# Optimization experiments

Measured on AMD Instinct MI355X. Metric: run time of the kernel, lower is better.

Reference implementation:

```python
import jax, jax.numpy as jnp
import numpy as np
from jax import lax


def _quadrature_weights(bw):
    # s2cnn-style Driscoll-Healy quadrature weights over beta, length 2*bw
    j = np.arange(2 * bw)
    k = np.arange(bw)
    theta = np.pi * (2 * j + 1) / (4 * bw)
    s = (np.sin(np.outer(2 * j + 1, 2 * k + 1) * np.pi / (4 * bw)) / (2 * k + 1)).sum(-1)
    return jnp.asarray((2.0 / bw) * np.sin(theta) * s, jnp.float32)


def _conv2d(x, W, b):
    y = lax.conv_general_dilated(x, W, (1, 1), 'SAME',
                                 dimension_numbers=('NCHW', 'OIHW', 'NCHW'))
    return y + b[None, :, None, None]


def setup_inputs() -> dict:
    key = jax.random.key(0)
    ks = jax.random.split(key, 8)
    b, n = 8, 32768
    res_pt, res_r = 32, 8
    inputs = jax.random.normal(ks[0], (b, n, 3), jnp.float32)
    return {
        'inputs': inputs,
        'scale': jnp.float32(3.0),      # max radius covered by radial bins
        'sigma': jnp.float32(0.5),      # gaussian width in grid units
        'A': jnp.float32(1.0),          # splat amplitude
        'inteval_comp': jnp.float32(0.5),
        'res_pt': res_pt,
        'res_r': res_r,
        'W_s2_1': 0.08 * jax.random.normal(ks[1], (32, 8, 3, 3), jnp.float32),
        'b_s2_1': jnp.zeros((32,), jnp.float32),
        'W_s2_2': 0.05 * jax.random.normal(ks[2], (64, 32, 3, 3), jnp.float32),
        'b_s2_2': jnp.zeros((64,), jnp.float32),
        'W_gamma': 0.1 * jax.random.normal(ks[3], (64, 32), jnp.float32),
        'W_c3_1': 0.05 * jax.random.normal(ks[4], (64, 128), jnp.float32),
        'b_c3_1': jnp.zeros((64,), jnp.float32),
        'W_c3_2': 0.05 * jax.random.normal(ks[5], (32, 64), jnp.float32),
        'b_c3_2': jnp.zeros((32,), jnp.float32),
    }


def reference(inputs, scale, sigma, A, inteval_comp, res_pt, res_r,
              W_s2_1, b_s2_1, W_s2_2, b_s2_2, W_gamma,
              W_c3_1, b_c3_1, W_c3_2, b_c3_2):
    b, n, _ = inputs.shape
    # ---- remap: cartesian -> spherical with min-radius clamp (utils.remap) ----
    x, y, z = inputs[..., 0], inputs[..., 1], inputs[..., 2]
    r = jnp.maximum(jnp.sqrt(x * x + y * y + z * z), 0.1)
    theta = jnp.arccos(jnp.clip(z / r, -1.0, 1.0))            # [0, pi]
    phi = jnp.arctan2(y, x) + np.pi                            # [0, 2pi)
    # ---- s2_gridding: gaussian-weighted point -> (theta,phi,r) grid scatter ----
    ct = theta / np.pi * res_pt                                # continuous bin coords
    cp = phi / (2 * np.pi) * res_pt
    cr = r / scale * res_r
    it = jnp.clip(jnp.floor(ct).astype(jnp.int32), 0, res_pt - 1)
    ip = jnp.clip(jnp.floor(cp).astype(jnp.int32), 0, res_pt - 1)
    ir = jnp.clip(jnp.floor(cr).astype(jnp.int32), 0, res_r - 1)
    d2 = ((ct - (it + inteval_comp)) ** 2
          + (cp - (ip + inteval_comp)) ** 2
          + (cr - (ir + inteval_comp)) ** 2)
    w = A * jnp.exp(-d2 / (2.0 * sigma * sigma))               # (b, n)
    vals = jnp.stack([w, w * x, w * y, w * z], axis=-1)        # (b, n, 4)
    bidx = jnp.arange(b, dtype=jnp.int32)[:, None] * jnp.ones((1, n), jnp.int32)
    flat = ((bidx * res_pt + it) * res_pt + ip) * res_r + ir   # (b, n)
    grid = jnp.zeros((b * res_pt * res_pt * res_r, 4), jnp.float32)
    grid = grid.at[flat.reshape(-1)].add(vals.reshape(-1, 4))
    grid = grid.reshape(b, res_pt, res_pt, res_r, 4)
    ft = jnp.transpose(grid[..., 0], (0, 3, 1, 2))             # (b, res_r, res_pt, res_pt)
    # ---- encoder_l1 (s2cnn_equators): S2 convs + gamma lift to SO3 grid ----
    h = jax.nn.relu(_conv2d(ft, W_s2_1, b_s2_1))
    h = jax.nn.relu(_conv2d(h, W_s2_2, b_s2_2))                # (b, 64, res_pt, res_pt)
    ft_grid = jnp.einsum('bcxy,cg->bcxyg', h, W_gamma)         # (b, 64, rp, rp, rp)
    # ---- so3_integrate: quadrature weight over beta, sum alpha/gamma ----
    wq = _quadrature_weights(res_pt // 2)                      # (res_pt,)
    ft_max = jnp.einsum('bcxyg,y->bc', ft_grid, wq)            # (b, 64)
    # ---- broadcast global feature, concat, pointwise conv3d head ----
    ft_max_ = jnp.broadcast_to(ft_max[:, :, None, None, None],
                               (b, ft_grid.shape[1], res_pt, res_pt, res_pt))
    cat = jnp.concatenate([ft_grid, ft_max_], axis=1)          # (b, 128, rp, rp, rp)
    h3 = jax.nn.relu(jnp.einsum('bcxyg,dc->bdxyg', cat, W_c3_1)
                     + b_c3_1[None, :, None, None, None])
    out = (jnp.einsum('bdxyg,ed->bexyg', h3, W_c3_2)
           + b_c3_2[None, :, None, None, None])                # (b, 32, rp, rp, rp)
    ft_g = out.reshape(b, out.shape[1], -1).max(-1)            # (b, 32)
    return (out, ft_g)
```

## Files before the change

kernel.cpp:

```cpp
#include <hip/hip_runtime.h>
#include <math.h>

#define PI_D 3.14159265358979323846
#define PI_F 3.14159265358979323846f

typedef _Float16 half8 __attribute__((ext_vector_type(8)));
typedef _Float16 half4v __attribute__((ext_vector_type(4)));
typedef float floatx4 __attribute__((ext_vector_type(4)));
#define MFMA16(a,b,c) __builtin_amdgcn_mfma_f32_16x16x32_f16(a,b,c,0,0,0)

__global__ void k_prep(const float* __restrict__ Wg, const float* __restrict__ Wc31,
                       const float* __restrict__ Wc32,
                       _Float16* __restrict__ VswH, _Float16* __restrict__ VswL,
                       _Float16* __restrict__ W2swH, _Float16* __restrict__ W2swL,
                       float* __restrict__ ft, float* __restrict__ WS,
                       float* __restrict__ wq, float* __restrict__ sgs) {
  int flat = blockIdx.x * 256 + threadIdx.x;
  {
    int jj = flat & 7;
    int l  = (flat >> 3) & 63;
    int rest = flat >> 9;
    int ks = rest & 1, mt = rest >> 1;
    int c = ks*32 + (l >> 4)*8 + jj;
    int m = mt*16 + (l & 15);
    int g = m >> 6, d = m & 63;
    float val = Wg[c*32 + g] * Wc31[d*128 + c];
    _Float16 hi = (_Float16)val;
    VswH[flat] = hi;
    VswL[flat] = (_Float16)(val - (float)hi);
  }
  if (flat < 2048) {
    int jj = flat & 7;
    int l  = (flat >> 3) & 63;
    int rest = flat >> 9;
    int ks = rest & 1, mt2 = rest >> 1;
    int e = mt2*16 + (l & 15);
    int d = ks*32 + (l >> 4)*8 + jj;
    float val = Wc32[e*64 + d];
    _Float16 hi = (_Float16)val;
    W2swH[flat] = hi;
    W2swL[flat] = (_Float16)(val - (float)hi);
  }
  if (flat < 16384) ((float4*)ft)[flat] = make_float4(0.f, 0.f, 0.f, 0.f);
  if (flat < 32) {
    double jj = 2.0*(double)flat + 1.0;
    double theta = PI_D * jj / 64.0;
    double s = 0.0;
    for (int k = 0; k < 16; ++k)
      s += sin(jj * (double)(2*k+1) * PI_D / 64.0) / (double)(2*k+1);
    wq[flat] = (float)((2.0/16.0) * sin(theta) * s);
  } else if (flat < 96) {
    int c = flat - 32;
    float s = 0.f;
    for (int g = 0; g < 32; ++g) s += Wg[c*32 + g];
    sgs[c] = s;
  } else if (flat < 608) {
    WS[flat - 96] = 0.f;
  }
}

__global__ void k_scatter(const float* __restrict__ inp,
                          const float* __restrict__ p_scale,
                          const float* __restrict__ p_sigma,
                          const float* __restrict__ p_A,
                          const float* __restrict__ p_ic,
                          float* __restrict__ ft) {
  int i = blockIdx.x * 256 + threadIdx.x;
  float scale = p_scale[0];
  float sigma = p_sigma[0];
  float A     = p_A[0];
  float icomp = p_ic[0];
  int b = i >> 15;
  float x = inp[i*3+0];
  float y = inp[i*3+1];
  float z = inp[i*3+2];
  float r = sqrtf(x*x + y*y + z*z);
  r = fmaxf(r, 0.1f);
  float ctv = fminf(fmaxf(z / r, -1.0f), 1.0f);
  float theta = acosf(ctv);
  float phi = atan2f(y, x) + PI_F;
  float ct = theta * (32.0f / PI_F);
  float cp = phi * (32.0f / (2.0f * PI_F));
  float cr = r / scale * 8.0f;
  int it = (int)floorf(ct); it = min(max(it, 0), 31);
  int ip = (int)floorf(cp); ip = min(max(ip, 0), 31);
  int ir = (int)floorf(cr); ir = min(max(ir, 0), 7);
  float dt = ct - ((float)it + icomp);
  float dp = cp - ((float)ip + icomp);
  float dr = cr - ((float)ir + icomp);
  float d2 = dt*dt + dp*dp + dr*dr;
  float w = A * expf(-d2 / (2.0f * sigma * sigma));
  atomicAdd(&ft[((b*8 + ir)*32 + it)*32 + ip], w);
}

__global__ __launch_bounds__(512) void k_conv12(
    const float* __restrict__ ft, const float* __restrict__ W1,
    const float* __restrict__ b1, const float* __restrict__ W2,
    const float* __restrict__ b2, const float* __restrict__ wq,
    float* __restrict__ h2, float* __restrict__ WS) {
  __shared__ __align__(16) float ftt[8][5][32];
  __shared__ __align__(16) float h1t[32][3][32];
  __shared__ __align__(16) float W1s[72*32];
  __shared__ __align__(16) float W2s[288*64];
  int blk = blockIdx.x;
  int b = blk >> 5, xt = blk & 31;
  int t = threadIdx.x;

  for (int idx = t; idx < 2304; idx += 512) {
    int oc2 = idx & 31, rest = idx >> 5;
    W1s[rest*32 + oc2] = W1[oc2*72 + rest];
  }
  for (int idx = t; idx < 18432; idx += 512) {
    int oc = idx & 63, rest = idx >> 6;
    W2s[rest*64 + oc] = W2[oc*288 + rest];
  }
  for (int idx = t; idx < 1280; idx += 512) {
    int y = idx & 31, xx = (idx >> 5) % 5, ic = idx / 160;
    int xg = xt + xx - 2;
    ftt[ic][xx][y] = ((unsigned)xg < 32u) ? ft[b*8192 + ic*1024 + xg*32 + y] : 0.f;
  }
  __syncthreads();

  {
    int y = t & 31, grp = t >> 5;
    float acc[2][3];
    float bb0 = b1[grp*2+0], bb1 = b1[grp*2+1];
#pragma unroll
    for (int xr = 0; xr < 3; ++xr) { acc[0][xr] = bb0; acc[1][xr] = bb1; }
    for (int ic = 0; ic < 8; ++ic) {
      float v[5][3];
#pragma unroll
      for (int dyi = 0; dyi < 3; ++dyi) {
        int yy = y + dyi - 1;
        bool ok = ((unsigned)yy < 32u);
        int yc = min(max(yy, 0), 31);
#pragma unroll
        for (int xx = 0; xx < 5; ++xx) {
          float tv = ftt[ic][xx][yc];
          v[xx][dyi] = ok ? tv : 0.f;
        }
      }
#pragma unroll
      for (int k = 0; k < 9; ++k) {
        float2 w = *(const float2*)&W1s[(ic*9 + k)*32 + grp*2];
        int dx = k / 3, dy = k % 3;
#pragma unroll
        for (int xr = 0; xr < 3; ++xr) {
          float vv = v[xr + dx][dy];
          acc[0][xr] = fmaf(vv, w.x, acc[0][xr]);
          acc[1][xr] = fmaf(vv, w.y, acc[1][xr]);
        }
      }
    }
#pragma unroll
    for (int xr = 0; xr < 3; ++xr) {
      int xg = xt + xr - 1;
      bool ok = ((unsigned)xg < 32u);
      h1t[grp*2+0][xr][y] = ok ? fmaxf(acc[0][xr], 0.f) : 0.f;
      h1t[grp*2+1][xr][y] = ok ? fmaxf(acc[1][xr], 0.f) : 0.f;
    }
  }
  __syncthreads();

  {
    int y = t & 31, og = t >> 5, oc0 = og*4;
    float a0 = b2[oc0+0], a1 = b2[oc0+1], a2 = b2[oc0+2], a3 = b2[oc0+3];
    for (int ic2 = 0; ic2 < 32; ++ic2) {
      float v[3][3];
#pragma unroll
      for (int dyi = 0; dyi < 3; ++dyi) {
        int yy = y + dyi - 1;
        bool ok = ((unsigned)yy < 32u);
        int yc = min(max(yy, 0), 31);
#pragma unroll
        for (int xxi = 0; xxi < 3; ++xxi) {
          float tv = h1t[ic2][xxi][yc];
          v[xxi][dyi] = ok ? tv : 0.f;
        }
      }
#pragma unroll
      for (int k = 0; k < 9; ++k) {
        float4 w = *(const float4*)&W2s[(ic2*9 + k)*64 + oc0];
        float vv = v[k/3][k%3];
        a0 = fmaf(vv, w.x, a0);
        a1 = fmaf(vv, w.y, a1);
        a2 = fmaf(vv, w.z, a2);
        a3 = fmaf(vv, w.w, a3);
      }
    }
    float r0 = fmaxf(a0, 0.f), r1 = fmaxf(a1, 0.f);
    float r2 = fmaxf(a2, 0.f), r3 = fmaxf(a3, 0.f);
    int pp = xt*32 + y;
    h2[(b*64 + oc0+0)*1024 + pp] = r0;
    h2[(b*64 + oc0+1)*1024 + pp] = r1;
    h2[(b*64 + oc0+2)*1024 + pp] = r2;
    h2[(b*64 + oc0+3)*1024 + pp] = r3;
    float wqv = wq[y];
    float s0 = r0*wqv, s1 = r1*wqv, s2 = r2*wqv, s3 = r3*wqv;
#pragma unroll
    for (int m = 1; m < 32; m <<= 1) {
      s0 += __shfl_xor(s0, m, 64);
      s1 += __shfl_xor(s1, m, 64);
      s2 += __shfl_xor(s2, m, 64);
      s3 += __shfl_xor(s3, m, 64);
    }
    if ((t & 31) == 0) {
      atomicAdd(&WS[b*64 + oc0+0], s0);
      atomicAdd(&WS[b*64 + oc0+1], s1);
      atomicAdd(&WS[b*64 + oc0+2], s2);
      atomicAdd(&WS[b*64 + oc0+3], s3);
    }
  }
}

__global__ __launch_bounds__(512, 4) void k_head(
    const float* __restrict__ h2, const float* __restrict__ WS,
    const float* __restrict__ sgs,
    const float* __restrict__ Wc31, const float* __restrict__ bc31,
    const float* __restrict__ bc32,
    const half8* __restrict__ VswH, const half8* __restrict__ VswL,
    const half8* __restrict__ W2swH, const half8* __restrict__ W2swL,
    float* __restrict__ out, float* __restrict__ blockmax) {
  __shared__ __align__(16) _Float16 h3H[512*72];
  __shared__ float Ks[64];
  __shared__ float vbuf2[128];
  int blk = blockIdx.x;
  int b = blk >> 6, x = (blk >> 1) & 31, h = blk & 1;
  int t = threadIdx.x;
  int lane = t & 63, w = t >> 6;
  int n16 = lane & 15, quad = lane >> 4;

  if (t < 64) {
    float acc = bc31[t];
    const float* wr = Wc31 + t*128 + 64;
    const float* wsb = WS + b*64;
    for (int c = 0; c < 64; ++c)
      acc = fmaf(wr[c], sgs[c]*wsb[c], acc);
    Ks[t] = acc;
  }

  half8 bh00, bh01, bh10, bh11, bl00, bl01, bl10, bl11;
  {
    const float* h2b = h2 + (size_t)b*64*1024 + x*32;
#pragma unroll
    for (int j = 0; j < 8; ++j) {
      int c0 = quad*8 + j;
      int c1 = 32 + c0;
      float f00 = h2b[c0*1024 + n16];
      float f01 = h2b[c1*1024 + n16];
      float f10 = h2b[c0*1024 + 16 + n16];
      float f11 = h2b[c1*1024 + 16 + n16];
      _Float16 g00 = (_Float16)f00, g01 = (_Float16)f01;
      _Float16 g10 = (_Float16)f10, g11 = (_Float16)f11;
      bh00[j] = g00;  bl00[j] = (_Float16)(f00 - (float)g00);
      bh01[j] = g01;  bl01[j] = (_Float16)(f01 - (float)g01);
      bh10[j] = g10;  bl10[j] = (_Float16)(f10 - (float)g10);
      bh11[j] = g11;  bl11[j] = (_Float16)(f11 - (float)g11);
    }
  }
  int mt2 = w & 1;
  half8 a2h0 = W2swH[(mt2*2 + 0)*64 + lane];
  half8 a2h1 = W2swH[(mt2*2 + 1)*64 + lane];
  half8 a2l0 = W2swL[(mt2*2 + 0)*64 + lane];
  half8 a2l1 = W2swL[(mt2*2 + 1)*64 + lane];
  float bias_e[4];
#pragma unroll
  for (int r = 0; r < 4; ++r) bias_e[r] = bc32[mt2*16 + quad*4 + r];
  __syncthreads();

  for (int i = 0; i < 8; ++i) {
    int mt = h*64 + w*8 + i;
    half8 ah0 = VswH[(mt*2 + 0)*64 + lane];
    half8 ah1 = VswH[(mt*2 + 1)*64 + lane];
    half8 al0 = VswL[(mt*2 + 0)*64 + lane];
    half8 al1 = VswL[(mt*2 + 1)*64 + lane];
    floatx4 acc0 = {0.f, 0.f, 0.f, 0.f};
    floatx4 acc1 = {0.f, 0.f, 0.f, 0.f};
    acc0 = MFMA16(ah0, bh00, acc0);  acc1 = MFMA16(ah0, bh10, acc1);
    acc0 = MFMA16(ah0, bl00, acc0);  acc1 = MFMA16(ah0, bl10, acc1);
    acc0 = MFMA16(al0, bh00, acc0);  acc1 = MFMA16(al0, bh10, acc1);
    acc0 = MFMA16(ah1, bh01, acc0);  acc1 = MFMA16(ah1, bh11, acc1);
    acc0 = MFMA16(ah1, bl01, acc0);  acc1 = MFMA16(ah1, bl11, acc1);
    acc0 = MFMA16(al1, bh01, acc0);  acc1 = MFMA16(al1, bh11, acc1);
    int g = mt >> 2, gl = g & 15;
    int dbase = (mt & 3)*16 + quad*4;
    float4 kv = *(const float4*)&Ks[dbase];
#pragma unroll
    for (int nt = 0; nt < 2; ++nt) {
      floatx4 a = nt ? acc1 : acc0;
      int y = nt*16 + n16;
      int rowc = y*16 + gl;
      int dsw = (dbase + y*8) & 63;
      half4v hv;
      hv[0] = (_Float16)fmaxf(a[0] + kv.x, 0.f);
      hv[1] = (_Float16)fmaxf(a[1] + kv.y, 0.f);
      hv[2] = (_Float16)fmaxf(a[2] + kv.z, 0.f);
      hv[3] = (_Float16)fmaxf(a[3] + kv.w, 0.f);
      *(half4v*)&h3H[rowc*72 + dsw] = hv;
    }
  }
  __syncthreads();
  float vmax[4] = {-3.4e38f, -3.4e38f, -3.4e38f, -3.4e38f};
  for (int i = 0; i < 8; ++i) {
    int nt2 = (w >> 1)*8 + i;
    int rowc = nt2*16 + n16;
    int dsw0 = (quad*8 + nt2*8) & 63;
    int dsw1 = (32 + quad*8 + nt2*8) & 63;
    half8 b2h0 = *(const half8*)&h3H[rowc*72 + dsw0];
    half8 b2h1 = *(const half8*)&h3H[rowc*72 + dsw1];
    floatx4 acc = {0.f, 0.f, 0.f, 0.f};
    acc = MFMA16(a2h0, b2h0, acc);
    acc = MFMA16(a2l0, b2h0, acc);
    acc = MFMA16(a2h1, b2h1, acc);
    acc = MFMA16(a2l1, b2h1, acc);
    int y = nt2, g = h*16 + n16;
    size_t base = (((size_t)(b*32 + mt2*16 + quad*4))*1024 + (size_t)(x*32 + y))*32 + g;
#pragma unroll
    for (int r = 0; r < 4; ++r) {
      float v = acc[r] + bias_e[r];
      out[base + (size_t)r*32768] = v;
      vmax[r] = fmaxf(vmax[r], v);
    }
  }
#pragma unroll
  for (int m = 1; m < 16; m <<= 1) {
#pragma unroll
    for (int r = 0; r < 4; ++r)
      vmax[r] = fmaxf(vmax[r], __shfl_xor(vmax[r], m, 64));
  }
  if (n16 == 0) {
#pragma unroll
    for (int r = 0; r < 4; ++r) vbuf2[w*16 + quad*4 + r] = vmax[r];
  }
  __syncthreads();
  if (t < 32) {
    int e = t, m2 = e >> 4, el = e & 15;
    float mm = fmaxf(fmaxf(vbuf2[(m2+0)*16 + el], vbuf2[(m2+2)*16 + el]),
                     fmaxf(vbuf2[(m2+4)*16 + el], vbuf2[(m2+6)*16 + el]));
    blockmax[blk*32 + e] = mm;
  }
}

__global__ void k_final(const float* __restrict__ blockmax, float* __restrict__ ftg) {
  int t = threadIdx.x;
  int b = t >> 5, e = t & 31;
  float m = -3.4e38f;
  for (int s = 0; s < 64; ++s) m = fmaxf(m, blockmax[(b*64 + s)*32 + e]);
  ftg[b*32 + e] = m;
}

extern "C" void kernel_launch(void* const* d_in, const int* in_sizes, int n_in,
                              void* d_out, int out_size, void* d_ws, size_t ws_size,
                              hipStream_t stream) {
  const float* inputs = (const float*)d_in[0];
  const float* scale  = (const float*)d_in[1];
  const float* sigma  = (const float*)d_in[2];
  const float* A      = (const float*)d_in[3];
  const float* icmp   = (const float*)d_in[4];
  const float* W1   = (const float*)d_in[7];
  const float* b1   = (const float*)d_in[8];
  const float* W2   = (const float*)d_in[9];
  const float* b2   = (const float*)d_in[10];
  const float* Wg   = (const float*)d_in[11];
  const float* Wc31 = (const float*)d_in[12];
  const float* bc31 = (const float*)d_in[13];
  const float* Wc32 = (const float*)d_in[14];
  const float* bc32 = (const float*)d_in[15];

  float* ws    = (float*)d_ws;
  float* ft    = ws;
  float* h2    = ws + 327680;
  float* WS    = ws + 851968;
  float* bmax  = ws + 852480;
  float* wq    = ws + 868864;
  float* sgs   = ws + 868896;
  _Float16* VswH  = (_Float16*)(ws + 868992);
  _Float16* VswL  = (_Float16*)(ws + 934528);
  _Float16* W2swH = (_Float16*)(ws + 1000064);
  _Float16* W2swL = (_Float16*)(ws + 1001088);
  float* out   = (float*)d_out;
  float* ftg   = out + 8388608;

  k_prep<<<512, 256, 0, stream>>>(Wg, Wc31, Wc32, VswH, VswL, W2swH, W2swL,
                                  ft, WS, wq, sgs);
  k_scatter<<<1024, 256, 0, stream>>>(inputs, scale, sigma, A, icmp, ft);
  k_conv12<<<256, 512, 0, stream>>>(ft, W1, b1, W2, b2, wq, h2, WS);
  k_head<<<512, 512, 0, stream>>>(h2, WS, sgs, Wc31, bc31, bc32,
                                  (const half8*)VswH, (const half8*)VswL,
                                  (const half8*)W2swH, (const half8*)W2swL,
                                  out, bmax);
  k_final<<<1, 256, 0, stream>>>(bmax, ftg);
}
```

Before: 175.5 us.

## Fold prep kernel into scatter/conv, pad LDS weights, split head blocks finer

Removes the separate k_prep launch. The ft buffer is now zeroed with a memset, the small setup work moves into block 0 of k_scatter, and the fp16 weight swizzling moves into k_conv12. Conv weights are now loaded from global memory coalesced and stored in LDS with padded strides (33/65) to avoid bank conflicts, at the cost of giving up vector LDS reads. k_head is split into 1024 blocks, each handling half the y range with half the LDS, and launch bounds rise to 8 blocks per SM for more occupancy. The final reduction and workspace offsets are adjusted to match.

```diff
diff --git a/kernel.cpp b/kernel.cpp
--- a/kernel.cpp
+++ b/kernel.cpp
@@ -8,64 +8,34 @@
 typedef _Float16 half4v __attribute__((ext_vector_type(4)));
 typedef float floatx4 __attribute__((ext_vector_type(4)));
 #define MFMA16(a,b,c) __builtin_amdgcn_mfma_f32_16x16x32_f16(a,b,c,0,0,0)
-
-__global__ void k_prep(const float* __restrict__ Wg, const float* __restrict__ Wc31,
-                       const float* __restrict__ Wc32,
-                       _Float16* __restrict__ VswH, _Float16* __restrict__ VswL,
-                       _Float16* __restrict__ W2swH, _Float16* __restrict__ W2swL,
-                       float* __restrict__ ft, float* __restrict__ WS,
-                       float* __restrict__ wq, float* __restrict__ sgs) {
-  int flat = blockIdx.x * 256 + threadIdx.x;
-  {
-    int jj = flat & 7;
-    int l  = (flat >> 3) & 63;
-    int rest = flat >> 9;
-    int ks = rest & 1, mt = rest >> 1;
-    int c = ks*32 + (l >> 4)*8 + jj;
-    int m = mt*16 + (l & 15);
-    int g = m >> 6, d = m & 63;
-    float val = Wg[c*32 + g] * Wc31[d*128 + c];
-    _Float16 hi = (_Float16)val;
-    VswH[flat] = hi;
-    VswL[flat] = (_Float16)(val - (float)hi);
-  }
-  if (flat < 2048) {
-    int jj = flat & 7;
-    int l  = (flat >> 3) & 63;
-    int rest = flat >> 9;
-    int ks = rest & 1, mt2 = rest >> 1;
-    int e = mt2*16 + (l & 15);
-    int d = ks*32 + (l >> 4)*8 + jj;
-    float val = Wc32[e*64 + d];
-    _Float16 hi = (_Float16)val;
-    W2swH[flat] = hi;
-    W2swL[flat] = (_Float16)(val - (float)hi);
-  }
-  if (flat < 16384) ((float4*)ft)[flat] = make_float4(0.f, 0.f, 0.f, 0.f);
-  if (flat < 32) {
-    double jj = 2.0*(double)flat + 1.0;
-    double theta = PI_D * jj / 64.0;
-    double s = 0.0;
-    for (int k = 0; k < 16; ++k)
-      s += sin(jj * (double)(2*k+1) * PI_D / 64.0) / (double)(2*k+1);
-    wq[flat] = (float)((2.0/16.0) * sin(theta) * s);
-  } else if (flat < 96) {
-    int c = flat - 32;
-    float s = 0.f;
-    for (int g = 0; g < 32; ++g) s += Wg[c*32 + g];
-    sgs[c] = s;
-  } else if (flat < 608) {
-    WS[flat - 96] = 0.f;
-  }
-}
 
 __global__ void k_scatter(const float* __restrict__ inp,
                           const float* __restrict__ p_scale,
                           const float* __restrict__ p_sigma,
                           const float* __restrict__ p_A,
                           const float* __restrict__ p_ic,
-                          float* __restrict__ ft) {
-  int i = blockIdx.x * 256 + threadIdx.x;
+                          const float* __restrict__ Wg,
+                          float* __restrict__ ft, float* __restrict__ wq,
+                          float* __restrict__ sgs, float* __restrict__ WS) {
+  int blk = blockIdx.x, t = threadIdx.x;
+  if (blk == 0) {
+    if (t < 32) {
+      double jj = 2.0*(double)t + 1.0;
+      double theta = PI_D * jj / 64.0;
+      double s = 0.0;
+      for (int k = 0; k < 16; ++k)
+        s += sin(jj * (double)(2*k+1) * PI_D / 64.0) / (double)(2*k+1);
+      wq[t] = (float)((2.0/16.0) * sin(theta) * s);
+    } else if (t < 96) {
+      int c = t - 32;
+      float s = 0.f;
+      for (int g = 0; g < 32; ++g) s += Wg[c*32 + g];
+      sgs[c] = s;
+    } else if (t < 224) {
+      ((float4*)WS)[t - 96] = make_float4(0.f, 0.f, 0.f, 0.f);
+    }
+  }
+  int i = blk * 256 + t;
   float scale = p_scale[0];
   float sigma = p_sigma[0];
   float A     = p_A[0];
@@ -97,22 +67,55 @@
     const float* __restrict__ ft, const float* __restrict__ W1,
     const float* __restrict__ b1, const float* __restrict__ W2,
     const float* __restrict__ b2, const float* __restrict__ wq,
+    const float* __restrict__ Wg, const float* __restrict__ Wc31,
+    const float* __restrict__ Wc32,
+    _Float16* __restrict__ VswH, _Float16* __restrict__ VswL,
+    _Float16* __restrict__ W2swH, _Float16* __restrict__ W2swL,
     float* __restrict__ h2, float* __restrict__ WS) {
   __shared__ __align__(16) float ftt[8][5][32];
   __shared__ __align__(16) float h1t[32][3][32];
-  __shared__ __align__(16) float W1s[72*32];
-  __shared__ __align__(16) float W2s[288*64];
+  __shared__ __align__(16) float W1s[72*33];
+  __shared__ __align__(16) float W2s[288*65];
   int blk = blockIdx.x;
   int b = blk >> 5, xt = blk & 31;
   int t = threadIdx.x;
 
+  {
+    int flat = blk * 512 + t;
+    int jj = flat & 7;
+    int l  = (flat >> 3) & 63;
+    int rest = flat >> 9;
+    int ks = rest & 1, mt = rest >> 1;
+    int c = ks*32 + (l >> 4)*8 + jj;
+    int m = mt*16 + (l & 15);
+    int g = m >> 6, d = m & 63;
+    float val = Wg[c*32 + g] * Wc31[d*128 + c];
+    _Float16 hi = (_Float16)val;
+    VswH[flat] = hi;
+    VswL[flat] = (_Float16)(val - (float)hi);
+    if (flat < 2048) {
+      int ks2 = rest & 1, mt2 = rest >> 1;
+      int e = mt2*16 + (l & 15);
+      int dd = ks2*32 + (l >> 4)*8 + jj;
+      float v2 = Wc32[e*64 + dd];
+      _Float16 h2i = (_Float16)v2;
+      W2swH[flat] = h2i;
+      W2swL[flat] = (_Float16)(v2 - (float)h2i);
+    }
+  }
+
   for (int idx = t; idx < 2304; idx += 512) {
-    int oc2 = idx & 31, rest = idx >> 5;
-    W1s[rest*32 + oc2] = W1[oc2*72 + rest];
-  }
-  for (int idx = t; idx < 18432; idx += 512) {
-    int oc = idx & 63, rest = idx >> 6;
-    W2s[rest*64 + oc] = W2[oc*288 + rest];
+    int oc2 = idx / 72, rest = idx % 72;
+    W1s[rest*33 + oc2] = W1[idx];
+  }
+  for (int idx = t; idx < 4608; idx += 512) {
+    float4 v4 = ((const float4*)W2)[idx];
+    int base = idx * 4;
+    int oc = base / 288, r0 = base % 288;
+    W2s[(r0+0)*65 + oc] = v4.x;
+    W2s[(r0+1)*65 + oc] = v4.y;
+    W2s[(r0+2)*65 + oc] = v4.z;
+    W2s[(r0+3)*65 + oc] = v4.w;
   }
   for (int idx = t; idx < 1280; idx += 512) {
     int y = idx & 31, xx = (idx >> 5) % 5, ic = idx / 160;
@@ -142,13 +145,14 @@
       }
 #pragma unroll
       for (int k = 0; k < 9; ++k) {
-        float2 w = *(const float2*)&W1s[(ic*9 + k)*32 + grp*2];
+        float w0 = W1s[(ic*9 + k)*33 + grp*2];
+        float w1 = W1s[(ic*9 + k)*33 + grp*2 + 1];
         int dx = k / 3, dy = k % 3;
 #pragma unroll
         for (int xr = 0; xr < 3; ++xr) {
           float vv = v[xr + dx][dy];
-          acc[0][xr] = fmaf(vv, w.x, acc[0][xr]);
-          acc[1][xr] = fmaf(vv, w.y, acc[1][xr]);
+          acc[0][xr] = fmaf(vv, w0, acc[0][xr]);
+          acc[1][xr] = fmaf(vv, w1, acc[1][xr]);
         }
       }
     }
@@ -180,12 +184,13 @@
       }
 #pragma unroll
       for (int k = 0; k < 9; ++k) {
-        float4 w = *(const float4*)&W2s[(ic2*9 + k)*64 + oc0];
+        int row = (ic2*9 + k)*65 + oc0;
+        float w0 = W2s[row+0], w1 = W2s[row+1], w2 = W2s[row+2], w3 = W2s[row+3];
         float vv = v[k/3][k%3];
-        a0 = fmaf(vv, w.x, a0);
-        a1 = fmaf(vv, w.y, a1);
-        a2 = fmaf(vv, w.z, a2);
-        a3 = fmaf(vv, w.w, a3);
+        a0 = fmaf(vv, w0, a0);
+        a1 = fmaf(vv, w1, a1);
+        a2 = fmaf(vv, w2, a2);
+        a3 = fmaf(vv, w3, a3);
       }
     }
     float r0 = fmaxf(a0, 0.f), r1 = fmaxf(a1, 0.f);
@@ -213,7 +218,7 @@
   }
 }
 
-__global__ __launch_bounds__(512, 4) void k_head(
+__global__ __launch_bounds__(512, 8) void k_head(
     const float* __restrict__ h2, const float* __restrict__ WS,
     const float* __restrict__ sgs,
     const float* __restrict__ Wc31, const float* __restrict__ bc31,
@@ -221,11 +226,11 @@
     const half8* __restrict__ VswH, const half8* __restrict__ VswL,
     const half8* __restrict__ W2swH, const half8* __restrict__ W2swL,
     float* __restrict__ out, float* __restrict__ blockmax) {
-  __shared__ __align__(16) _Float16 h3H[512*72];
+  __shared__ __align__(16) _Float16 h3H[256*72];
   __shared__ float Ks[64];
   __shared__ float vbuf2[128];
   int blk = blockIdx.x;
-  int b = blk >> 6, x = (blk >> 1) & 31, h = blk & 1;
+  int b = blk >> 7, x = (blk >> 2) & 31, h = (blk >> 1) & 1, yh = blk & 1;
   int t = threadIdx.x;
   int lane = t & 63, w = t >> 6;
   int n16 = lane & 15, quad = lane >> 4;
@@ -239,23 +244,17 @@
     Ks[t] = acc;
   }
 
-  half8 bh00, bh01, bh10, bh11, bl00, bl01, bl10, bl11;
+  half8 bh0, bh1, bl0, bl1;
   {
-    const float* h2b = h2 + (size_t)b*64*1024 + x*32;
+    const float* h2b = h2 + (size_t)b*64*1024 + x*32 + yh*16;
 #pragma unroll
     for (int j = 0; j < 8; ++j) {
       int c0 = quad*8 + j;
-      int c1 = 32 + c0;
-      float f00 = h2b[c0*1024 + n16];
-      float f01 = h2b[c1*1024 + n16];
-      float f10 = h2b[c0*1024 + 16 + n16];
-      float f11 = h2b[c1*1024 + 16 + n16];
-      _Float16 g00 = (_Float16)f00, g01 = (_Float16)f01;
-      _Float16 g10 = (_Float16)f10, g11 = (_Float16)f11;
-      bh00[j] = g00;  bl00[j] = (_Float16)(f00 - (float)g00);
-      bh01[j] = g01;  bl01[j] = (_Float16)(f01 - (float)g01);
-      bh10[j] = g10;  bl10[j] = (_Float16)(f10 - (float)g10);
-      bh11[j] = g11;  bl11[j] = (_Float16)(f11 - (float)g11);
+      float f0 = h2b[c0*1024 + n16];
+      float f1 = h2b[(32 + c0)*1024 + n16];
+      _Float16 g0 = (_Float16)f0, g1 = (_Float16)f1;
+      bh0[j] = g0;  bl0[j] = (_Float16)(f0 - (float)g0);
+      bh1[j] = g1;  bl1[j] = (_Float16)(f1 - (float)g1);
     }
   }
   int mt2 = w & 1;
@@ -274,38 +273,34 @@
     half8 ah1 = VswH[(mt*2 + 1)*64 + lane];
     half8 al0 = VswL[(mt*2 + 0)*64 + lane];
     half8 al1 = VswL[(mt*2 + 1)*64 + lane];
-    floatx4 acc0 = {0.f, 0.f, 0.f, 0.f};
-    floatx4 acc1 = {0.f, 0.f, 0.f, 0.f};
-    acc0 = MFMA16(ah0, bh00, acc0);  acc1 = MFMA16(ah0, bh10, acc1);
-    acc0 = MFMA16(ah0, bl00, acc0);  acc1 = MFMA16(ah0, bl10, acc1);
-    acc0 = MFMA16(al0, bh00, acc0);  acc1 = MFMA16(al0, bh10, acc1);
-    acc0 = MFMA16(ah1, bh01, acc0);  acc1 = MFMA16(ah1, bh11, acc1);
-    acc0 = MFMA16(ah1, bl01, acc0);  acc1 = MFMA16(ah1, bl11, acc1);
-    acc0 = MFMA16(al1, bh01, acc0);  acc1 = MFMA16(al1, bh11, acc1);
+    floatx4 acc = {0.f, 0.f, 0.f, 0.f};
+    acc = MFMA16(ah0, bh0, acc);
+    acc = MFMA16(ah0, bl0, acc);
+    acc = MFMA16(al0, bh0, acc);
+    acc = MFMA16(ah1, bh1, acc);
+    acc = MFMA16(ah1, bl1, acc);
+    acc = MFMA16(al1, bh1, acc);
     int g = mt >> 2, gl = g & 15;
     int dbase = (mt & 3)*16 + quad*4;
     float4 kv = *(const float4*)&Ks[dbase];
-#pragma unroll
-    for (int nt = 0; nt < 2; ++nt) {
-      floatx4 a = nt ? acc1 : acc0;
-      int y = nt*16 + n16;
-      int rowc = y*16 + gl;
-      int dsw = (dbase + y*8) & 63;
-      half4v hv;
-      hv[0] = (_Float16)fmaxf(a[0] + kv.x, 0.f);
-      hv[1] = (_Float16)fmaxf(a[1] + kv.y, 0.f);
-      hv[2] = (_Float16)fmaxf(a[2] + kv.z, 0.f);
-      hv[3] = (_Float16)fmaxf(a[3] + kv.w, 0.f);
-      *(half4v*)&h3H[rowc*72 + dsw] = hv;
-    }
+    int y_l = n16;
+    int rowc = y_l*16 + gl;
+    int dsw = (dbase + y_l*8) & 63;
+    half4v hv;
+    hv[0] = (_Float16)fmaxf(acc[0] + kv.x, 0.f);
+    hv[1] = (_Float16)fmaxf(acc[1] + kv.y, 0.f);
+    hv[2] = (_Float16)fmaxf(acc[2] + kv.z, 0.f);
+    hv[3] = (_Float16)fmaxf(acc[3] + kv.w, 0.f);
+    *(half4v*)&h3H[rowc*72 + dsw] = hv;
   }
   __syncthreads();
   float vmax[4] = {-3.4e38f, -3.4e38f, -3.4e38f, -3.4e38f};
-  for (int i = 0; i < 8; ++i) {
-    int nt2 = (w >> 1)*8 + i;
-    int rowc = nt2*16 + n16;
-    int dsw0 = (quad*8 + nt2*8) & 63;
-    int dsw1 = (32 + quad*8 + nt2*8) & 63;
+  int grp = w >> 1;
+  for (int i = 0; i < 4; ++i) {
+    int y_l = grp*4 + i;
+    int rowc = y_l*16 + n16;
+    int dsw0 = (quad*8 + y_l*8) & 63;
+    int dsw1 = (32 + quad*8 + y_l*8) & 63;
     half8 b2h0 = *(const half8*)&h3H[rowc*72 + dsw0];
     half8 b2h1 = *(const half8*)&h3H[rowc*72 + dsw1];
     floatx4 acc = {0.f, 0.f, 0.f, 0.f};
@@ -313,7 +308,7 @@
     acc = MFMA16(a2l0, b2h0, acc);
     acc = MFMA16(a2h1, b2h1, acc);
     acc = MFMA16(a2l1, b2h1, acc);
-    int y = nt2, g = h*16 + n16;
+    int y = yh*16 + y_l, g = h*16 + n16;
     size_t base = (((size_t)(b*32 + mt2*16 + quad*4))*1024 + (size_t)(x*32 + y))*32 + g;
 #pragma unroll
     for (int r = 0; r < 4; ++r) {
@@ -345,7 +340,7 @@
   int t = threadIdx.x;
   int b = t >> 5, e = t & 31;
   float m = -3.4e38f;
-  for (int s = 0; s < 64; ++s) m = fmaxf(m, blockmax[(b*64 + s)*32 + e]);
+  for (int s = 0; s < 128; ++s) m = fmaxf(m, blockmax[(b*128 + s)*32 + e]);
   ftg[b*32 + e] = m;
 }
 
@@ -372,22 +367,23 @@
   float* h2    = ws + 327680;
   float* WS    = ws + 851968;
   float* bmax  = ws + 852480;
-  float* wq    = ws + 868864;
-  float* sgs   = ws + 868896;
-  _Float16* VswH  = (_Float16*)(ws + 868992);
-  _Float16* VswL  = (_Float16*)(ws + 934528);
-  _Float16* W2swH = (_Float16*)(ws + 1000064);
-  _Float16* W2swL = (_Float16*)(ws + 1001088);
+  float* wq    = ws + 885248;
+  float* sgs   = ws + 885280;
+  _Float16* VswH  = (_Float16*)(ws + 885344);
+  _Float16* VswL  = (_Float16*)(ws + 950880);
+  _Float16* W2swH = (_Float16*)(ws + 1016416);
+  _Float16* W2swL = (_Float16*)(ws + 1017440);
   float* out   = (float*)d_out;
   float* ftg   = out + 8388608;
 
-  k_prep<<<512, 256, 0, stream>>>(Wg, Wc31, Wc32, VswH, VswL, W2swH, W2swL,
-                                  ft, WS, wq, sgs);
-  k_scatter<<<1024, 256, 0, stream>>>(inputs, scale, sigma, A, icmp, ft);
-  k_conv12<<<256, 512, 0, stream>>>(ft, W1, b1, W2, b2, wq, h2, WS);
-  k_head<<<512, 512, 0, stream>>>(h2, WS, sgs, Wc31, bc31, bc32,
-                                  (const half8*)VswH, (const half8*)VswL,
-                                  (const half8*)W2swH, (const half8*)W2swL,
-                                  out, bmax);
+  hipMemsetAsync(ft, 0, 65536*sizeof(float), stream);
+  k_scatter<<<1024, 256, 0, stream>>>(inputs, scale, sigma, A, icmp, Wg,
+                                      ft, wq, sgs, WS);
+  k_conv12<<<256, 512, 0, stream>>>(ft, W1, b1, W2, b2, wq, Wg, Wc31, Wc32,
+                                    VswH, VswL, W2swH, W2swL, h2, WS);
+  k_head<<<1024, 512, 0, stream>>>(h2, WS, sgs, Wc31, bc31, bc32,
+                                   (const half8*)VswH, (const half8*)VswL,
+                                   (const half8*)W2swH, (const half8*)W2swL,
+                                   out, bmax);
   k_final<<<1, 256, 0, stream>>>(bmax, ftg);
 }
```

Measured after the change: 208.2 us. 18.6% more time.
